# Kernel tuning notes

Measured on AMD Instinct MI355X. Metric: run time of the kernel, lower is better.

Reference implementation:

```python
import jax, jax.numpy as jnp
import numpy as np
import math

D1 = D2 = D3 = 256
B, S = 2, 384
SCALE = math.sqrt((D1 + D2 + D3) / 3)  # arc_norm scale


def setup_inputs() -> dict:
    key = jax.random.key(0)
    k1, k2, k3, kw = jax.random.split(key, 4)
    matrix_1 = jax.random.normal(k1, (B, S, D1), dtype=jnp.float32)
    matrix_2 = jax.random.normal(k2, (B, S, D2), dtype=jnp.float32)
    matrix_3 = jax.random.normal(k3, (B, S, D3), dtype=jnp.float32)
    # xavier-uniform-like scale for the trilinear tensor parameter
    W = jax.random.normal(kw, (D1, D2, D3), dtype=jnp.float32) * 0.02
    return {"matrix_1": matrix_1, "matrix_2": matrix_2, "matrix_3": matrix_3, "W": W}


def reference(matrix_1, matrix_2, matrix_3, W):
    _, s, _ = matrix_1.shape
    # mode == 'sib': upper-triangular (diag=1) mask over the (j, k) dims
    mask = jnp.triu(jnp.ones((s, s), dtype=bool), k=1)[None, None, :, :]  # [1,1,S,S]
    # Faithful reproduction of the original einsum chain (note: subscripts are
    # exactly as in the torch module, including the independent sum indices).
    v1U = jnp.einsum('bix,pqr->biqr', matrix_1, W)          # [B,S,D2,D3]
    v1Uv2 = jnp.einsum('biqr,bjx->bijr', v1U, matrix_2)      # [B,S,S,D3]
    scores = jnp.einsum('bkx,bijr->bijk', matrix_3, v1Uv2)   # [B,S,S,S]
    scores = jnp.where(mask, scores, 0.0)                    # masked_fill(~mask, 0)
    return scores / SCALE                                    # activation = Passthrough
```

## Files before the change

### kernel.cpp

```cpp
#include <hip/hip_runtime.h>

#define SS 384
#define BB 2
#define DD 256
#define NPART 1024

#define WS_PART 16
#define WS_M1 2048
#define WS_M2 2816
#define WS_M3 3584

__global__ void rowsum_kernel(const float* __restrict__ m1,
                              const float* __restrict__ m2,
                              const float* __restrict__ m3,
                              float* __restrict__ ws) {
    int wave = (blockIdx.x * blockDim.x + threadIdx.x) >> 6;
    int lane = threadIdx.x & 63;
    if (wave >= 3 * BB * SS) return;
    const float* src;
    float* dst;
    if (wave < BB * SS)          { src = m1 + (size_t)wave * DD;               dst = ws + WS_M1 + wave; }
    else if (wave < 2 * BB * SS) { src = m2 + (size_t)(wave - BB * SS) * DD;   dst = ws + WS_M2 + (wave - BB * SS); }
    else                         { src = m3 + (size_t)(wave - 2 * BB * SS) * DD; dst = ws + WS_M3 + (wave - 2 * BB * SS); }
    float4 v = ((const float4*)src)[lane];
    float s = (v.x + v.y) + (v.z + v.w);
    #pragma unroll
    for (int off = 32; off; off >>= 1) s += __shfl_down(s, off, 64);
    if (lane == 0) *dst = s;
}

__global__ void wsum_part_kernel(const float* __restrict__ W, float* __restrict__ ws) {
    __shared__ float sm[4];
    const float4* W4 = (const float4*)W;
    const unsigned n4 = (DD * DD * DD) / 4;
    float s = 0.f;
    for (unsigned i = blockIdx.x * blockDim.x + threadIdx.x; i < n4; i += gridDim.x * blockDim.x) {
        float4 v = W4[i];
        s += (v.x + v.y) + (v.z + v.w);
    }
    #pragma unroll
    for (int off = 32; off; off >>= 1) s += __shfl_down(s, off, 64);
    int lane = threadIdx.x & 63, w = threadIdx.x >> 6;
    if (lane == 0) sm[w] = s;
    __syncthreads();
    if (threadIdx.x == 0) ws[WS_PART + blockIdx.x] = (sm[0] + sm[1]) + (sm[2] + sm[3]);
}

__global__ void wsum_final_kernel(float* __restrict__ ws) {
    __shared__ float sm[4];
    __shared__ float smTot;
    float s = 0.f;
    for (int i = threadIdx.x; i < NPART; i += 256) s += ws[WS_PART + i];
    #pragma unroll
    for (int off = 32; off; off >>= 1) s += __shfl_down(s, off, 64);
    int lane = threadIdx.x & 63, w = threadIdx.x >> 6;
    if (lane == 0) sm[w] = s;
    __syncthreads();
    if (threadIdx.x == 0) {
        float t = (sm[0] + sm[1]) + (sm[2] + sm[3]);
        ws[0] = t;
        smTot = t;
    }
    __syncthreads();
    float c = smTot * (1.0f / 16.0f);
    for (int i = threadIdx.x; i < BB * SS; i += 256) ws[WS_M3 + i] *= c;
}

__global__ void writer_kernel(const float* __restrict__ ws, float* __restrict__ out) {
    const float* m1s = ws + WS_M1;
    const float* m2s = ws + WS_M2;
    const float* f3  = ws + WS_M3;
    const unsigned K4 = SS / 4;
    const unsigned total4 = BB * SS * SS * K4;
    const unsigned stride = gridDim.x * blockDim.x;
    for (unsigned n = blockIdx.x * blockDim.x + threadIdx.x; n < total4; n += stride) {
        unsigned k4 = n % K4;
        unsigned t  = n / K4;
        unsigned j  = t % SS;
        unsigned t2 = t / SS;
        unsigned i  = t2 % SS;
        unsigned b  = t2 / SS;
        float c = m1s[b * SS + i] * m2s[b * SS + j];
        float4 f = ((const float4*)(f3 + b * SS))[k4];
        int k0 = (int)(k4 * 4);
        int jj = (int)j;
        float4 o;
        o.x = (k0 + 0 > jj) ? c * f.x : 0.f;
        o.y = (k0 + 1 > jj) ? c * f.y : 0.f;
        o.z = (k0 + 2 > jj) ? c * f.z : 0.f;
        o.w = (k0 + 3 > jj) ? c * f.w : 0.f;
        ((float4*)out)[n] = o;
    }
}

extern "C" void kernel_launch(void* const* d_in, const int* in_sizes, int n_in,
                              void* d_out, int out_size, void* d_ws, size_t ws_size,
                              hipStream_t stream) {
    const float* m1 = (const float*)d_in[0];
    const float* m2 = (const float*)d_in[1];
    const float* m3 = (const float*)d_in[2];
    const float* W  = (const float*)d_in[3];
    float* out = (float*)d_out;
    float* ws  = (float*)d_ws;

    rowsum_kernel<<<576, 256, 0, stream>>>(m1, m2, m3, ws);
    wsum_part_kernel<<<NPART, 256, 0, stream>>>(W, ws);
    wsum_final_kernel<<<1, 256, 0, stream>>>(ws);
    writer_kernel<<<2048, 256, 0, stream>>>(ws, out);
}
```

Measured before the change: 112.8 us.

## Fuse rowsum and W partial-sum kernels; restructure writer to one block per row

The row-sum and W partial-sum kernels are merged into a single launch, with block index selecting the role, which removes one kernel launch and its gap. The writer kernel moves from a grid-stride loop with per-element div/mod index decoding to one 384-thread block per (b,i) row. Each thread keeps its f3 float4 and c1 in registers and loops over j with a stride of four. This cuts integer index arithmetic and redundant loads in the output-bandwidth-bound writer, at the cost of a fixed grid of 768 blocks.

```diff
diff --git a/kernel.cpp b/kernel.cpp
--- a/kernel.cpp
+++ b/kernel.cpp
@@ -10,40 +10,41 @@
 #define WS_M2 2816
 #define WS_M3 3584
 
-__global__ void rowsum_kernel(const float* __restrict__ m1,
+__global__ void stage1_kernel(const float* __restrict__ m1,
                               const float* __restrict__ m2,
                               const float* __restrict__ m3,
+                              const float* __restrict__ W,
                               float* __restrict__ ws) {
-    int wave = (blockIdx.x * blockDim.x + threadIdx.x) >> 6;
-    int lane = threadIdx.x & 63;
-    if (wave >= 3 * BB * SS) return;
-    const float* src;
-    float* dst;
-    if (wave < BB * SS)          { src = m1 + (size_t)wave * DD;               dst = ws + WS_M1 + wave; }
-    else if (wave < 2 * BB * SS) { src = m2 + (size_t)(wave - BB * SS) * DD;   dst = ws + WS_M2 + (wave - BB * SS); }
-    else                         { src = m3 + (size_t)(wave - 2 * BB * SS) * DD; dst = ws + WS_M3 + (wave - 2 * BB * SS); }
-    float4 v = ((const float4*)src)[lane];
-    float s = (v.x + v.y) + (v.z + v.w);
-    #pragma unroll
-    for (int off = 32; off; off >>= 1) s += __shfl_down(s, off, 64);
-    if (lane == 0) *dst = s;
-}
-
-__global__ void wsum_part_kernel(const float* __restrict__ W, float* __restrict__ ws) {
-    __shared__ float sm[4];
-    const float4* W4 = (const float4*)W;
-    const unsigned n4 = (DD * DD * DD) / 4;
-    float s = 0.f;
-    for (unsigned i = blockIdx.x * blockDim.x + threadIdx.x; i < n4; i += gridDim.x * blockDim.x) {
-        float4 v = W4[i];
-        s += (v.x + v.y) + (v.z + v.w);
+    if (blockIdx.x < NPART) {
+        __shared__ float sm[4];
+        const float4* W4 = (const float4*)W;
+        const unsigned n4 = (DD * DD * DD) / 4;
+        float s = 0.f;
+        for (unsigned i = blockIdx.x * blockDim.x + threadIdx.x; i < n4; i += NPART * 256) {
+            float4 v = W4[i];
+            s += (v.x + v.y) + (v.z + v.w);
+        }
+        #pragma unroll
+        for (int off = 32; off; off >>= 1) s += __shfl_down(s, off, 64);
+        int lane = threadIdx.x & 63, w = threadIdx.x >> 6;
+        if (lane == 0) sm[w] = s;
+        __syncthreads();
+        if (threadIdx.x == 0) ws[WS_PART + blockIdx.x] = (sm[0] + sm[1]) + (sm[2] + sm[3]);
+    } else {
+        int wave = (int)(blockIdx.x - NPART) * 4 + (int)(threadIdx.x >> 6);
+        int lane = threadIdx.x & 63;
+        if (wave >= 3 * BB * SS) return;
+        const float* src;
+        float* dst;
+        if (wave < BB * SS)          { src = m1 + (size_t)wave * DD;                 dst = ws + WS_M1 + wave; }
+        else if (wave < 2 * BB * SS) { src = m2 + (size_t)(wave - BB * SS) * DD;     dst = ws + WS_M2 + (wave - BB * SS); }
+        else                         { src = m3 + (size_t)(wave - 2 * BB * SS) * DD; dst = ws + WS_M3 + (wave - 2 * BB * SS); }
+        float4 v = ((const float4*)src)[lane];
+        float s = (v.x + v.y) + (v.z + v.w);
+        #pragma unroll
+        for (int off = 32; off; off >>= 1) s += __shfl_down(s, off, 64);
+        if (lane == 0) *dst = s;
     }
-    #pragma unroll
-    for (int off = 32; off; off >>= 1) s += __shfl_down(s, off, 64);
-    int lane = threadIdx.x & 63, w = threadIdx.x >> 6;
-    if (lane == 0) sm[w] = s;
-    __syncthreads();
-    if (threadIdx.x == 0) ws[WS_PART + blockIdx.x] = (sm[0] + sm[1]) + (sm[2] + sm[3]);
 }
 
 __global__ void wsum_final_kernel(float* __restrict__ ws) {
@@ -66,30 +67,28 @@
     for (int i = threadIdx.x; i < BB * SS; i += 256) ws[WS_M3 + i] *= c;
 }
 
-__global__ void writer_kernel(const float* __restrict__ ws, float* __restrict__ out) {
-    const float* m1s = ws + WS_M1;
-    const float* m2s = ws + WS_M2;
-    const float* f3  = ws + WS_M3;
-    const unsigned K4 = SS / 4;
-    const unsigned total4 = BB * SS * SS * K4;
-    const unsigned stride = gridDim.x * blockDim.x;
-    for (unsigned n = blockIdx.x * blockDim.x + threadIdx.x; n < total4; n += stride) {
-        unsigned k4 = n % K4;
-        unsigned t  = n / K4;
-        unsigned j  = t % SS;
-        unsigned t2 = t / SS;
-        unsigned i  = t2 % SS;
-        unsigned b  = t2 / SS;
-        float c = m1s[b * SS + i] * m2s[b * SS + j];
-        float4 f = ((const float4*)(f3 + b * SS))[k4];
-        int k0 = (int)(k4 * 4);
-        int jj = (int)j;
+__global__ void __launch_bounds__(384) writer_kernel(const float* __restrict__ ws,
+                                                     float* __restrict__ out) {
+    int bi = blockIdx.x;
+    int b  = bi / SS;
+    const float* m2s = ws + WS_M2 + b * SS;
+    const float* f3  = ws + WS_M3 + b * SS;
+    float c1 = ws[WS_M1 + bi];
+    int t    = threadIdx.x;
+    int jrow = t / 96;
+    int k4   = t - jrow * 96;
+    float4 f = ((const float4*)f3)[k4];
+    int k0 = k4 * 4;
+    float4* dst = (float4*)out + (size_t)bi * (SS * SS / 4);
+    #pragma unroll 2
+    for (int j = jrow; j < SS; j += 4) {
+        float cj = c1 * m2s[j];
         float4 o;
-        o.x = (k0 + 0 > jj) ? c * f.x : 0.f;
-        o.y = (k0 + 1 > jj) ? c * f.y : 0.f;
-        o.z = (k0 + 2 > jj) ? c * f.z : 0.f;
-        o.w = (k0 + 3 > jj) ? c * f.w : 0.f;
-        ((float4*)out)[n] = o;
+        o.x = (k0 + 0 > j) ? cj * f.x : 0.f;
+        o.y = (k0 + 1 > j) ? cj * f.y : 0.f;
+        o.z = (k0 + 2 > j) ? cj * f.z : 0.f;
+        o.w = (k0 + 3 > j) ? cj * f.w : 0.f;
+        dst[j * 96 + k4] = o;
     }
 }
 
@@ -103,8 +102,7 @@
     float* out = (float*)d_out;
     float* ws  = (float*)d_ws;
 
-    rowsum_kernel<<<576, 256, 0, stream>>>(m1, m2, m3, ws);
-    wsum_part_kernel<<<NPART, 256, 0, stream>>>(W, ws);
+    stage1_kernel<<<NPART + 576, 256, 0, stream>>>(m1, m2, m3, W, ws);
     wsum_final_kernel<<<1, 256, 0, stream>>>(ws);
-    writer_kernel<<<2048, 256, 0, stream>>>(ws, out);
+    writer_kernel<<<BB * SS, 384, 0, stream>>>(ws, out);
 }
```

After: 111.4 us. Within noise of the previous version (-1.2%).
